# Kernel tuning notes

Hardware: AMD Instinct MI355X
Metric: run time of the kernel (lower is better)

The kernel has to match this reference:

```python
import jax, jax.numpy as jnp
import numpy as np

B, S, N = 64, 256, 512


def setup_inputs() -> dict:
    key = jax.random.key(0)
    ks = jax.random.split(key, 8)
    x = jax.random.normal(ks[0], (B, S, N), dtype=jnp.float32)
    # sparse adjacency, no self loops (module assumes adj has no self-loop)
    adj = (jax.random.uniform(ks[1], (N, N)) < 0.05).astype(jnp.float32)
    adj = adj * (1.0 - jnp.eye(N, dtype=jnp.float32))
    W = jax.random.uniform(ks[2], (N, N), dtype=jnp.float32)  # torch.rand init
    parent_node_weigh = jax.random.uniform(ks[3], (N,), dtype=jnp.float32)
    bound = 1.0 / np.sqrt(N)  # torch Linear default init
    Wq_w = jax.random.uniform(ks[4], (N, N), minval=-bound, maxval=bound, dtype=jnp.float32)
    Wq_b = jax.random.uniform(ks[5], (N,), minval=-bound, maxval=bound, dtype=jnp.float32)
    Wk_w = jax.random.uniform(ks[6], (N, N), minval=-bound, maxval=bound, dtype=jnp.float32)
    Wk_b = jax.random.uniform(ks[7], (N,), minval=-bound, maxval=bound, dtype=jnp.float32)
    return {"x": x, "adj": adj, "W": W, "parent_node_weigh": parent_node_weigh,
            "Wq_w": Wq_w, "Wq_b": Wq_b, "Wk_w": Wk_w, "Wk_b": Wk_b}


def reference(x, adj, W, parent_node_weigh, Wq_w, Wq_b, Wk_w, Wk_b):
    # x: (B,S,N). Q,K = Linear(x).permute(0,2,1) -> (B,N,S)
    Q = jnp.einsum('bsk,nk->bns', x, Wq_w) + Wq_b[None, :, None]
    K = jnp.einsum('bsk,nk->bns', x, Wk_w) + Wk_b[None, :, None]
    xt = jnp.transpose(x, (0, 2, 1))  # (B,N,S)
    n = adj.shape[0]
    # Algebraic equivalent of the repeat/mask/matmul/bmm chain:
    # Att[b,m,n] = adj[m,n] * sum_j W[m,j] * adj[j,n] * <K[b,j,:], Q[b,n,:]>
    S_kq = jnp.einsum('bjs,bns->bjn', K, Q)  # (B,N,N)
    Att = adj * jnp.einsum('mj,bjn->bmn', W, adj[:, :, None].transpose(2, 0, 1)[0][None] * S_kq if False else adj[None, :, :] * S_kq)
    Att = Att + jnp.diag(parent_node_weigh)[None, :, :]
    cycle_adj = jnp.eye(n, dtype=adj.dtype) + adj
    Att = jax.nn.softmax(Att, axis=1) * cycle_adj  # softmax over dim=1 (torch dim=1)
    agg_x = jnp.einsum('bmn,bms->bns', Att, xt)  # Att^T @ x
    return (agg_x, Att)
```

## Files before the change

### kernel.cpp

```cpp
#include <hip/hip_runtime.h>
#include <hip/hip_fp16.h>
#include <cstdint>
#include <cmath>

#define BB 64
#define SS 256
#define NN 512
#define MAXC 64

typedef float f32x4 __attribute__((ext_vector_type(4)));
typedef _Float16 half8 __attribute__((ext_vector_type(8)));

__device__ __forceinline__ unsigned short f2h(float f) {
  return __half_as_ushort(__float2half(f));
}
__device__ __forceinline__ float h2f(unsigned short u) {
  return __half2float(__ushort_as_half(u));
}

__device__ __forceinline__ void gload_lds16(const void* g, void* s) {
  __builtin_amdgcn_global_load_lds(
      (const __attribute__((address_space(1))) uint32_t*)g,
      (__attribute__((address_space(3))) uint32_t*)s, 16, 0, 0);
}

__global__ __launch_bounds__(256) void k_prep0(const float* __restrict__ adj,
                                               int* __restrict__ col_idx,
                                               int* __restrict__ col_cnt,
                                               const float* __restrict__ Wq,
                                               const float* __restrict__ Wk,
                                               unsigned short* __restrict__ Wqp,
                                               unsigned short* __restrict__ Wkp) {
  if (blockIdx.x < 128) {
    const int n = blockIdx.x * 4 + (threadIdx.x >> 6);
    const int lane = threadIdx.x & 63;
    int cnt = 0;
    for (int m0 = 0; m0 < NN; m0 += 64) {
      const int m = m0 + lane;
      const float a = adj[(size_t)m * NN + n];
      unsigned long long mask = __ballot(a != 0.0f);
      const int prefix = __popcll(mask & ((1ull << lane) - 1ull));
      if (a != 0.0f && cnt + prefix < MAXC) col_idx[n * MAXC + cnt + prefix] = m;
      cnt += __popcll(mask);
    }
    if (lane == 0) col_cnt[n] = (cnt > MAXC) ? MAXC : cnt;
  } else {
    const int n = blockIdx.x - 128;
    const int half = threadIdx.x >> 7;
    const float* src = half ? Wk : Wq;
    unsigned short* dst = half ? Wkp : Wqp;
    const int k = (threadIdx.x & 127) * 4;
    float4 v = *(const float4*)(src + (size_t)n * NN + k);
    ushort4 o;
    o.x = f2h(v.x); o.y = f2h(v.y); o.z = f2h(v.z); o.w = f2h(v.w);
    *(ushort4*)(dst + (size_t)n * 512 + k) = o;
  }
}

__global__ __launch_bounds__(256) void k_wsub(const float* __restrict__ W,
                                              const int* __restrict__ col_idx,
                                              const int* __restrict__ col_cnt,
                                              int* __restrict__ col_off,
                                              float* __restrict__ Wsub) {
  const int n = blockIdx.x;
  const int t = threadIdx.x;
  const int wave = t >> 6, lane = t & 63;
  __shared__ int lsh[MAXC];
  __shared__ int preSh;
  const int c = col_cnt[n];
  if (wave == 0) {
    int pre = 0;
#pragma unroll
    for (int i0 = 0; i0 < NN; i0 += 64) {
      const int i = i0 + lane;
      const int cc = col_cnt[i];
      pre += (i < n) ? cc * cc : 0;
    }
#pragma unroll
    for (int off = 32; off; off >>= 1) pre += __shfl_xor(pre, off);
    if (lane == 0) { col_off[n] = pre; preSh = pre; }
    if (lane < c) lsh[lane] = col_idx[n * MAXC + lane];
  }
  __syncthreads();
  if (lane < c) {
    const float* Wm = W + (size_t)lsh[lane] * NN;
    float* dst = Wsub + preSh + lane;
    for (int ji = wave; ji < c; ji += 4)
      dst[(size_t)ji * c] = Wm[lsh[ji]];
  }
}

__global__ __launch_bounds__(256) void k_xprep(const float* __restrict__ x,
                                               unsigned short* __restrict__ xp,
                                               float* __restrict__ Att) {
  const int t = threadIdx.x;
  const size_t base = ((size_t)blockIdx.x * 256 + t) * 4;
  float4 v = *(const float4*)(x + base);
  ushort4 o;
  o.x = f2h(v.x); o.y = f2h(v.y); o.z = f2h(v.z); o.w = f2h(v.w);
  *(ushort4*)(xp + base) = o;
  f32x4* dst = (f32x4*)(Att + (size_t)blockIdx.x * 2048);
  const f32x4 z = (f32x4)0.0f;
  dst[t] = z;
  dst[t + 256] = z;
}

__global__ __launch_bounds__(256, 2) void k_lin2(const unsigned short* __restrict__ Wqp,
                                                 const unsigned short* __restrict__ Wkp,
                                                 const float* __restrict__ bq,
                                                 const float* __restrict__ bk,
                                                 const unsigned short* __restrict__ xp,
                                                 unsigned short* __restrict__ Qt,
                                                 unsigned short* __restrict__ Kt) {
  __shared__ __align__(16) char sm[49152];
  const int t = threadIdx.x;
  const int w = t >> 6, l = t & 63;
  const int id = blockIdx.x;
  const int xcd = id & 7, sub = id >> 3;
  const int bn0 = (xcd * 16 + (sub >> 2)) * 128;
  const int bm0 = (sub & 3) * 128;

  const int swz = (((l & 3) ^ ((l >> 3) & 3))) * 16;
  const char* srcb[6];
  char* dstb[6];
#pragma unroll
  for (int i = 0; i < 6; i++) {
    const int ch = w * 6 + i;
    const int panel = ch >> 3, rowgrp = ch & 7;
    const int row = rowgrp * 16 + (l >> 2);
    const char* g0 = (panel == 0) ? (const char*)Wqp
                   : (panel == 1) ? (const char*)Wkp : (const char*)xp;
    const int gr = ((panel == 2) ? bn0 : bm0) + row;
    srcb[i] = g0 + (size_t)gr * 1024 + swz;
    dstb[i] = sm + panel * 8192 + rowgrp * 1024 + l * 16;
  }

  const int fr = l & 15, fg = l >> 4;
  const int mrow = (w >> 1) * 64, ncol = (w & 1) * 64;
  const int slot = (fg ^ ((fr >> 1) & 3)) * 16;
  int offQ[4], offK[4], offB[4];
#pragma unroll
  for (int fm = 0; fm < 4; fm++) {
    offQ[fm] = (mrow + fm * 16 + fr) * 64 + slot;
    offK[fm] = 8192 + (mrow + fm * 16 + fr) * 64 + slot;
    offB[fm] = 16384 + (ncol + fm * 16 + fr) * 64 + slot;
  }

  f32x4 accq[4][4], acck[4][4];
#pragma unroll
  for (int i = 0; i < 4; i++)
#pragma unroll
    for (int j = 0; j < 4; j++) { accq[i][j] = (f32x4)0.0f; acck[i][j] = (f32x4)0.0f; }

#pragma unroll
  for (int i = 0; i < 6; i++) gload_lds16(srcb[i], dstb[i]);
  __syncthreads();

  int cur = 0;
  for (int kk = 0; kk < 16; kk++) {
    if (kk + 1 < 16) {
      const int ko = (kk + 1) * 64;
      const int boff = (cur ^ 1) * 24576;
#pragma unroll
      for (int i = 0; i < 6; i++)
        gload_lds16(srcb[i] + ko, dstb[i] + boff);
    }
    const char* base = sm + cur * 24576;
    half8 afq[4], afk[4];
#pragma unroll
    for (int fm = 0; fm < 4; fm++) {
      afq[fm] = *(const half8*)(base + offQ[fm]);
      afk[fm] = *(const half8*)(base + offK[fm]);
    }
#pragma unroll
    for (int fn = 0; fn < 4; fn++) {
      const half8 bv = *(const half8*)(base + offB[fn]);
#pragma unroll
      for (int fm = 0; fm < 4; fm++) {
        accq[fm][fn] = __builtin_amdgcn_mfma_f32_16x16x32_f16(afq[fm], bv, accq[fm][fn], 0, 0, 0);
        acck[fm][fn] = __builtin_amdgcn_mfma_f32_16x16x32_f16(afk[fm], bv, acck[fm][fn], 0, 0, 0);
      }
    }
    __syncthreads();
    cur ^= 1;
  }

  const int b = bn0 >> 8;
  const int sbase = (bn0 & 255) + ncol;
#pragma unroll
  for (int fm = 0; fm < 4; fm++) {
#pragma unroll
    for (int q = 0; q < 4; q++) {
      const int n = bm0 + mrow + fm * 16 + fg * 4 + q;
      const float bvq = bq[n];
      const float bvk = bk[n];
#pragma unroll
      for (int fn = 0; fn < 4; fn++) {
        const int s = sbase + fn * 16 + fr;
        Qt[((size_t)b * NN + n) * SS + s] = f2h(accq[fm][fn][q] + bvq);
        Kt[((size_t)b * NN + n) * SS + s] = f2h(acck[fm][fn][q] + bvk);
      }
    }
  }
}

__global__ __launch_bounds__(256, 2) void k_gram(const unsigned short* __restrict__ Qt,
                                                 const unsigned short* __restrict__ Kt,
                                                 unsigned short* __restrict__ ST) {
  __shared__ __align__(16) char sm[32768];
  const int t = threadIdx.x;
  const int w = t >> 6, l = t & 63;
  const int id = blockIdx.x;
  const int xcd = id & 7, rest = id >> 3;
  const int batch = (xcd << 3) + (rest >> 4);
  const int tile = rest & 15;
  const int m0 = (tile >> 2) * 128;
  const int n0 = (tile & 3) * 128;

  const int swz = (((l & 3) ^ ((l >> 3) & 3))) * 16;
  const char* srcb[4];
  char* dstb[4];
#pragma unroll
  for (int i = 0; i < 4; i++) {
    const int ch = w * 4 + i;
    const int panel = ch >> 3, rowgrp = ch & 7;
    const int row = rowgrp * 16 + (l >> 2);
    const char* g0 = panel ? (const char*)Kt : (const char*)Qt;
    const int gr = (panel ? n0 : m0) + row;
    srcb[i] = g0 + ((size_t)batch * 512 + gr) * 512 + swz;
    dstb[i] = sm + panel * 8192 + rowgrp * 1024 + l * 16;
  }

  const int fr = l & 15, fg = l >> 4;
  const int mrow = (w >> 1) * 64, ncol = (w & 1) * 64;
  const int slot = (fg ^ ((fr >> 1) & 3)) * 16;
  int offA[4], offB[4];
#pragma unroll
  for (int fm = 0; fm < 4; fm++) {
    offA[fm] = (mrow + fm * 16 + fr) * 64 + slot;
    offB[fm] = 8192 + (ncol + fm * 16 + fr) * 64 + slot;
  }

  f32x4 acc[4][4];
#pragma unroll
  for (int i = 0; i < 4; i++)
#pragma unroll
    for (int j = 0; j < 4; j++) acc[i][j] = (f32x4)0.0f;

#pragma unroll
  for (int i = 0; i < 4; i++) gload_lds16(srcb[i], dstb[i]);
  __syncthreads();

  int cur = 0;
  for (int kk = 0; kk < 8; kk++) {
    if (kk + 1 < 8) {
      const int ko = (kk + 1) * 64;
      const int boff = (cur ^ 1) * 16384;
#pragma unroll
      for (int i = 0; i < 4; i++)
        gload_lds16(srcb[i] + ko, dstb[i] + boff);
    }
    const char* base = sm + cur * 16384;
    half8 af[4];
#pragma unroll
    for (int fm = 0; fm < 4; fm++)
      af[fm] = *(const half8*)(base + offA[fm]);
#pragma unroll
    for (int fn = 0; fn < 4; fn++) {
      const half8 bv = *(const half8*)(base + offB[fn]);
#pragma unroll
      for (int fm = 0; fm < 4; fm++)
        acc[fm][fn] = __builtin_amdgcn_mfma_f32_16x16x32_f16(af[fm], bv, acc[fm][fn], 0, 0, 0);
    }
    __syncthreads();
    cur ^= 1;
  }

  unsigned short* STb = ST + (size_t)batch * NN * NN;
#pragma unroll
  for (int fm = 0; fm < 4; fm++) {
#pragma unroll
    for (int q = 0; q < 4; q++) {
      const int n = m0 + mrow + fm * 16 + fg * 4 + q;
#pragma unroll
      for (int fn = 0; fn < 4; fn++) {
        const int j = n0 + ncol + fn * 16 + fr;
        STb[(size_t)n * NN + j] = f2h(acc[fm][fn][q]);
      }
    }
  }
}

__global__ __launch_bounds__(256) void k_fused(const unsigned short* __restrict__ ST,
                                               const float* __restrict__ Wsub,
                                               const float* __restrict__ pnw,
                                               const int* __restrict__ col_idx,
                                               const int* __restrict__ col_cnt,
                                               const int* __restrict__ col_off,
                                               float* __restrict__ Att,
                                               unsigned short* __restrict__ Att2) {
  const int id = blockIdx.x;
  const int xcd = id & 7;
  const int r = id >> 3;
  const int n = r & 511;
  const int bgrp = r >> 9;
  const int t = threadIdx.x;
  const int wave = t >> 6, lane = t & 63;
  const int b = (xcd << 3) + (bgrp << 2) + wave;

  __shared__ int   lsh[MAXC + 1];
  __shared__ float Wsh[MAXC * MAXC];
  __shared__ float vsh[4][MAXC];
  __shared__ unsigned short ush[4][NN];

  const int c = col_cnt[n];

  unsigned short stv = 0;
  if (lane < c) {
    const int myIdx = col_idx[n * MAXC + lane];
    stv = ST[((size_t)b * NN + n) * NN + myIdx];
  }

#pragma unroll
  for (int j = 0; j < 8; j++) ush[wave][lane * 8 + j] = 0;

  if (t < c) lsh[t] = col_idx[n * MAXC + t];
  if (t == c) lsh[c] = n;
  {
    const int cc = c * c;
    const float* Wp = Wsub + col_off[n];
    for (int i = t; i < cc; i += 256) Wsh[i] = Wp[i];
  }
  __syncthreads();

  if (lane < c) vsh[wave][lane] = h2f(stv);

  float aval = 0.0f;
  if (lane < c) {
    for (int ji = 0; ji < c; ji++)
      aval += Wsh[ji * c + lane] * vsh[wave][ji];
  }

  const float dlg = pnw[n];
  float mval = (lane < c) ? aval : -INFINITY;
#pragma unroll
  for (int off = 32; off; off >>= 1) mval = fmaxf(mval, __shfl_xor(mval, off));
  const float colmax = fmaxf(mval, fmaxf(dlg, 0.0f));
  const float e = (lane < c) ? __expf(aval - colmax) : 0.0f;
  float sum = e;
#pragma unroll
  for (int off = 32; off; off >>= 1) sum += __shfl_xor(sum, off);
  const float denom = sum + __expf(dlg - colmax)
                    + (float)(NN - c - 1) * __expf(-colmax);
  const float inv = 1.0f / denom;

  float* Acol = Att + (size_t)b * NN * NN + n;
  if (lane < c) {
    const float attv = e * inv;
    Acol[(size_t)lsh[lane] * NN] = attv;
    ush[wave][lsh[lane]] = f2h(attv);
  }
  if (lane == c) {
    const float dv = __expf(dlg - colmax) * inv;
    Acol[(size_t)n * NN] = dv;
    ush[wave][n] = f2h(dv);
  }

  uint32_t pk[4];
#pragma unroll
  for (int j = 0; j < 4; j++) {
    const uint32_t lo = ush[wave][lane * 8 + j * 2];
    const uint32_t hi = ush[wave][lane * 8 + j * 2 + 1];
    pk[j] = lo | (hi << 16);
  }
  uint4 o = make_uint4(pk[0], pk[1], pk[2], pk[3]);
  *(uint4*)((char*)Att2 + ((size_t)b * NN + n) * 1024 + lane * 16) = o;
}

__global__ __launch_bounds__(256, 2) void k_agg(const unsigned short* __restrict__ Att2,
                                                const unsigned short* __restrict__ xp,
                                                float* __restrict__ agg) {
  __shared__ __align__(16) char sm[32768];
  const int t = threadIdx.x;
  const int w = t >> 6, l = t & 63;
  const int id = blockIdx.x;
  const int xcd = id & 7, rest = id >> 3;
  const int batch = (xcd << 3) + (rest >> 3);
  const int tile = rest & 7;
  const int m0 = (tile >> 1) * 128;
  const int s0 = (tile & 1) * 128;

  const int swz = (((l & 3) ^ ((l >> 3) & 3))) * 16;
  const char* srcb[4];
  char* dstb[4];
#pragma unroll
  for (int i = 0; i < 4; i++) {
    const int ch = w * 4 + i;
    const int panel = ch >> 3, rowgrp = ch & 7;
    const int row = rowgrp * 16 + (l >> 2);
    const char* g0 = panel ? (const char*)xp : (const char*)Att2;
    const size_t gr = panel ? ((size_t)batch * SS + s0 + row)
                            : ((size_t)batch * NN + m0 + row);
    srcb[i] = g0 + gr * 1024 + swz;
    dstb[i] = sm + panel * 8192 + rowgrp * 1024 + l * 16;
  }

  const int fr = l & 15, fg = l >> 4;
  const int mrow = (w >> 1) * 64, ncol = (w & 1) * 64;
  const int slot = (fg ^ ((fr >> 1) & 3)) * 16;
  int offA[4], offB[4];
#pragma unroll
  for (int fm = 0; fm < 4; fm++) {
    offA[fm] = (mrow + fm * 16 + fr) * 64 + slot;
    offB[fm] = 8192 + (ncol + fm * 16 + fr) * 64 + slot;
  }

  f32x4 acc[4][4];
#pragma unroll
  for (int i = 0; i < 4; i++)
#pragma unroll
    for (int j = 0; j < 4; j++) acc[i][j] = (f32x4)0.0f;

#pragma unroll
  for (int i = 0; i < 4; i++) gload_lds16(srcb[i], dstb[i]);
  __syncthreads();

  int cur = 0;
  for (int kk = 0; kk < 16; kk++) {
    if (kk + 1 < 16) {
      const int ko = (kk + 1) * 64;
      const int boff = (cur ^ 1) * 16384;
#pragma unroll
      for (int i = 0; i < 4; i++)
        gload_lds16(srcb[i] + ko, dstb[i] + boff);
    }
    const char* base = sm + cur * 16384;
    half8 af[4];
#pragma unroll
    for (int fm = 0; fm < 4; fm++)
      af[fm] = *(const half8*)(base + offA[fm]);
#pragma unroll
    for (int fn = 0; fn < 4; fn++) {
      const half8 bv = *(const half8*)(base + offB[fn]);
#pragma unroll
      for (int fm = 0; fm < 4; fm++)
        acc[fm][fn] = __builtin_amdgcn_mfma_f32_16x16x32_f16(af[fm], bv, acc[fm][fn], 0, 0, 0);
    }
    __syncthreads();
    cur ^= 1;
  }

  float* ab = agg + (size_t)batch * NN * SS;
#pragma unroll
  for (int fm = 0; fm < 4; fm++) {
#pragma unroll
    for (int q = 0; q < 4; q++) {
      const int n = m0 + mrow + fm * 16 + fg * 4 + q;
#pragma unroll
      for (int fn = 0; fn < 4; fn++) {
        const int s = s0 + ncol + fn * 16 + fr;
        ab[(size_t)n * SS + s] = acc[fm][fn][q];
      }
    }
  }
}

extern "C" void kernel_launch(void* const* d_in, const int* in_sizes, int n_in,
                              void* d_out, int out_size, void* d_ws, size_t ws_size,
                              hipStream_t stream) {
  const float* x    = (const float*)d_in[0];
  const float* adj  = (const float*)d_in[1];
  const float* W    = (const float*)d_in[2];
  const float* pnw  = (const float*)d_in[3];
  const float* Wq_w = (const float*)d_in[4];
  const float* Wq_b = (const float*)d_in[5];
  const float* Wk_w = (const float*)d_in[6];
  const float* Wk_b = (const float*)d_in[7];

  float* agg = (float*)d_out;
  float* Att = (float*)d_out + (size_t)BB * NN * SS;

  char* p = (char*)d_ws;
  unsigned short* xp  = (unsigned short*)p; p += (size_t)BB * SS * 512 * 2;
  unsigned short* Wqp = (unsigned short*)p; p += (size_t)NN * 512 * 2;
  unsigned short* Wkp = (unsigned short*)p; p += (size_t)NN * 512 * 2;
  unsigned short* Qt  = (unsigned short*)p; p += (size_t)BB * NN * SS * 2;
  unsigned short* Kt  = (unsigned short*)p; p += (size_t)BB * NN * SS * 2;
  unsigned short* ST  = (unsigned short*)p; p += (size_t)BB * NN * NN * 2;
  unsigned short* At2 = (unsigned short*)p; p += (size_t)BB * NN * NN * 2;
  float* Wsub = (float*)p; p += (size_t)NN * MAXC * MAXC * 4;
  int* col_idx = (int*)p; p += (size_t)NN * MAXC * 4;
  int* col_cnt = (int*)p; p += NN * 4;
  int* col_off = (int*)p;

  k_prep0<<<dim3(640), dim3(256), 0, stream>>>(adj, col_idx, col_cnt,
                                               Wq_w, Wk_w, Wqp, Wkp);
  k_wsub<<<dim3(NN), dim3(256), 0, stream>>>(W, col_idx, col_cnt, col_off, Wsub);
  k_xprep<<<dim3(8192), dim3(256), 0, stream>>>(x, xp, Att);

  k_lin2<<<dim3(512), dim3(256), 0, stream>>>(Wqp, Wkp, Wq_b, Wk_b, xp, Qt, Kt);
  k_gram<<<dim3(1024), dim3(256), 0, stream>>>(Qt, Kt, ST);
  k_fused<<<dim3(8192), dim3(256), 0, stream>>>(ST, Wsub, pnw,
                                                col_idx, col_cnt, col_off,
                                                Att, At2);
  k_agg<<<dim3(512), dim3(256), 0, stream>>>(At2, xp, agg);
}
```

Baseline: 111.3 us.

## Merge x-prep into prep kernel and widen gram/agg tiles to 128x256

Folds the x fp16 conversion and Att zeroing into the prep kernel, removing one launch. Doubles the N-dimension tile in the gram and aggregation GEMMs to 128x256 (8 fragments per wave), halving their grid sizes and reusing the A panel across more columns. In exchange the accumulator register count doubles and LDS use rises to 48KB. This may cut occupancy, and 256 blocks for k_agg could underfill the GPU's compute units.

```diff
diff --git a/kernel.cpp b/kernel.cpp
--- a/kernel.cpp
+++ b/kernel.cpp
@@ -24,15 +24,19 @@
       (__attribute__((address_space(3))) uint32_t*)s, 16, 0, 0);
 }
 
-__global__ __launch_bounds__(256) void k_prep0(const float* __restrict__ adj,
-                                               int* __restrict__ col_idx,
-                                               int* __restrict__ col_cnt,
-                                               const float* __restrict__ Wq,
-                                               const float* __restrict__ Wk,
-                                               unsigned short* __restrict__ Wqp,
-                                               unsigned short* __restrict__ Wkp) {
-  if (blockIdx.x < 128) {
-    const int n = blockIdx.x * 4 + (threadIdx.x >> 6);
+__global__ __launch_bounds__(256) void k_prep(const float* __restrict__ adj,
+                                              int* __restrict__ col_idx,
+                                              int* __restrict__ col_cnt,
+                                              const float* __restrict__ Wq,
+                                              const float* __restrict__ Wk,
+                                              unsigned short* __restrict__ Wqp,
+                                              unsigned short* __restrict__ Wkp,
+                                              const float* __restrict__ x,
+                                              unsigned short* __restrict__ xp,
+                                              float* __restrict__ Att) {
+  const int bid = blockIdx.x;
+  if (bid < 128) {
+    const int n = bid * 4 + (threadIdx.x >> 6);
     const int lane = threadIdx.x & 63;
     int cnt = 0;
     for (int m0 = 0; m0 < NN; m0 += 64) {
@@ -44,8 +48,8 @@
       cnt += __popcll(mask);
     }
     if (lane == 0) col_cnt[n] = (cnt > MAXC) ? MAXC : cnt;
-  } else {
-    const int n = blockIdx.x - 128;
+  } else if (bid < 640) {
+    const int n = bid - 128;
     const int half = threadIdx.x >> 7;
     const float* src = half ? Wk : Wq;
     unsigned short* dst = half ? Wkp : Wqp;
@@ -54,6 +58,18 @@
     ushort4 o;
     o.x = f2h(v.x); o.y = f2h(v.y); o.z = f2h(v.z); o.w = f2h(v.w);
     *(ushort4*)(dst + (size_t)n * 512 + k) = o;
+  } else {
+    const int q = bid - 640;
+    const int t = threadIdx.x;
+    const size_t base = ((size_t)q * 256 + t) * 4;
+    float4 v = *(const float4*)(x + base);
+    ushort4 o;
+    o.x = f2h(v.x); o.y = f2h(v.y); o.z = f2h(v.z); o.w = f2h(v.w);
+    *(ushort4*)(xp + base) = o;
+    f32x4* dst = (f32x4*)(Att + (size_t)q * 2048);
+    const f32x4 z = (f32x4)0.0f;
+    dst[t] = z;
+    dst[t + 256] = z;
   }
 }
 
@@ -88,21 +104,6 @@
     for (int ji = wave; ji < c; ji += 4)
       dst[(size_t)ji * c] = Wm[lsh[ji]];
   }
-}
-
-__global__ __launch_bounds__(256) void k_xprep(const float* __restrict__ x,
-                                               unsigned short* __restrict__ xp,
-                                               float* __restrict__ Att) {
-  const int t = threadIdx.x;
-  const size_t base = ((size_t)blockIdx.x * 256 + t) * 4;
-  float4 v = *(const float4*)(x + base);
-  ushort4 o;
-  o.x = f2h(v.x); o.y = f2h(v.y); o.z = f2h(v.z); o.w = f2h(v.w);
-  *(ushort4*)(xp + base) = o;
-  f32x4* dst = (f32x4*)(Att + (size_t)blockIdx.x * 2048);
-  const f32x4 z = (f32x4)0.0f;
-  dst[t] = z;
-  dst[t + 256] = z;
 }
 
 __global__ __launch_bounds__(256, 2) void k_lin2(const unsigned short* __restrict__ Wqp,
@@ -207,66 +208,68 @@
 __global__ __launch_bounds__(256, 2) void k_gram(const unsigned short* __restrict__ Qt,
                                                  const unsigned short* __restrict__ Kt,
                                                  unsigned short* __restrict__ ST) {
-  __shared__ __align__(16) char sm[32768];
+  __shared__ __align__(16) char sm[49152];
   const int t = threadIdx.x;
   const int w = t >> 6, l = t & 63;
   const int id = blockIdx.x;
   const int xcd = id & 7, rest = id >> 3;
-  const int batch = (xcd << 3) + (rest >> 4);
-  const int tile = rest & 15;
-  const int m0 = (tile >> 2) * 128;
-  const int n0 = (tile & 3) * 128;
+  const int batch = (xcd << 3) + (rest >> 3);
+  const int tile = rest & 7;
+  const int m0 = (tile >> 1) * 128;
+  const int j0 = (tile & 1) * 256;
 
   const int swz = (((l & 3) ^ ((l >> 3) & 3))) * 16;
-  const char* srcb[4];
-  char* dstb[4];
-#pragma unroll
-  for (int i = 0; i < 4; i++) {
-    const int ch = w * 4 + i;
-    const int panel = ch >> 3, rowgrp = ch & 7;
+  const char* srcb[6];
+  char* dstb[6];
+#pragma unroll
+  for (int i = 0; i < 6; i++) {
+    const int ch = w * 6 + i;
+    const int panel = (ch >= 8) ? 1 : 0;
+    const int rowgrp = panel ? (ch - 8) : ch;
     const int row = rowgrp * 16 + (l >> 2);
     const char* g0 = panel ? (const char*)Kt : (const char*)Qt;
-    const int gr = (panel ? n0 : m0) + row;
+    const int gr = (panel ? j0 : m0) + row;
     srcb[i] = g0 + ((size_t)batch * 512 + gr) * 512 + swz;
     dstb[i] = sm + panel * 8192 + rowgrp * 1024 + l * 16;
   }
 
   const int fr = l & 15, fg = l >> 4;
-  const int mrow = (w >> 1) * 64, ncol = (w & 1) * 64;
+  const int mrow = (w >> 1) * 64, jcol = (w & 1) * 128;
   const int slot = (fg ^ ((fr >> 1) & 3)) * 16;
-  int offA[4], offB[4];
-#pragma unroll
-  for (int fm = 0; fm < 4; fm++) {
+  int offA[4], offB[8];
+#pragma unroll
+  for (int fm = 0; fm < 4; fm++)
     offA[fm] = (mrow + fm * 16 + fr) * 64 + slot;
-    offB[fm] = 8192 + (ncol + fm * 16 + fr) * 64 + slot;
-  }
-
-  f32x4 acc[4][4];
+#pragma unroll
+  for (int fn = 0; fn < 8; fn++)
+    offB[fn] = 8192 + (jcol + fn * 16 + fr) * 64 + slot;
+
+  f32x4 acc[4][8];
 #pragma unroll
   for (int i = 0; i < 4; i++)
 #pragma unroll
-    for (int j = 0; j < 4; j++) acc[i][j] = (f32x4)0.0f;
-
-#pragma unroll
-  for (int i = 0; i < 4; i++) gload_lds16(srcb[i], dstb[i]);
+    for (int j = 0; j < 8; j++) acc[i][j] = (f32x4)0.0f;
+
+#pragma unroll
+  for (int i = 0; i < 6; i++) gload_lds16(srcb[i], dstb[i]);
   __syncthreads();
 
   int cur = 0;
   for (int kk = 0; kk < 8; kk++) {
     if (kk + 1 < 8) {
       const int ko = (kk + 1) * 64;
-      const int boff = (cur ^ 1) * 16384;
-#pragma unroll
-      for (int i = 0; i < 4; i++)
+      const int boff = (cur ^ 1) * 24576;
+#pragma unroll
+      for (int i = 0; i < 6; i++)
         gload_lds16(srcb[i] + ko, dstb[i] + boff);
     }
-    const char* base = sm + cur * 16384;
+    const char* base = sm + cur * 24576;
     half8 af[4];
 #pragma unroll
     for (int fm = 0; fm < 4; fm++)
       af[fm] = *(const half8*)(base + offA[fm]);
 #pragma unroll
-    for (int fn = 0; fn < 4; fn++) {
+    for (int fn = 0; fn < 8; fn++) {
       const half8 bv = *(const half8*)(base + offB[fn]);
 #pragma unroll
       for (int fm = 0; fm < 4; fm++)
@@ -283,8 +286,8 @@
     for (int q = 0; q < 4; q++) {
       const int n = m0 + mrow + fm * 16 + fg * 4 + q;
 #pragma unroll
-      for (int fn = 0; fn < 4; fn++) {
-        const int j = n0 + ncol + fn * 16 + fr;
+      for (int fn = 0; fn < 8; fn++) {
+        const int j = j0 + jcol + fn * 16 + fr;
         STb[(size_t)n * NN + j] = f2h(acc[fm][fn][q]);
       }
     }
@@ -380,67 +383,67 @@
 __global__ __launch_bounds__(256, 2) void k_agg(const unsigned short* __restrict__ Att2,
                                                 const unsigned short* __restrict__ xp,
                                                 float* __restrict__ agg) {
-  __shared__ __align__(16) char sm[32768];
+  __shared__ __align__(16) char sm[49152];
   const int t = threadIdx.x;
   const int w = t >> 6, l = t & 63;
   const int id = blockIdx.x;
   const int xcd = id & 7, rest = id >> 3;
-  const int batch = (xcd << 3) + (rest >> 3);
-  const int tile = rest & 7;
-  const int m0 = (tile >> 1) * 128;
-  const int s0 = (tile & 1) * 128;
+  const int batch = (xcd << 3) + (rest >> 2);
+  const int m0 = (rest & 3) * 128;
 
   const int swz = (((l & 3) ^ ((l >> 3) & 3))) * 16;
-  const char* srcb[4];
-  char* dstb[4];
-#pragma unroll
-  for (int i = 0; i < 4; i++) {
-    const int ch = w * 4 + i;
-    const int panel = ch >> 3, rowgrp = ch & 7;
+  const char* srcb[6];
+  char* dstb[6];
+#pragma unroll
+  for (int i = 0; i < 6; i++) {
+    const int ch = w * 6 + i;
+    const int panel = (ch >= 8) ? 1 : 0;
+    const int rowgrp = panel ? (ch - 8) : ch;
     const int row = rowgrp * 16 + (l >> 2);
     const char* g0 = panel ? (const char*)xp : (const char*)Att2;
-    const size_t gr = panel ? ((size_t)batch * SS + s0 + row)
+    const size_t gr = panel ? ((size_t)batch * SS + row)
                             : ((size_t)batch * NN + m0 + row);
     srcb[i] = g0 + gr * 1024 + swz;
     dstb[i] = sm + panel * 8192 + rowgrp * 1024 + l * 16;
   }
 
   const int fr = l & 15, fg = l >> 4;
-  const int mrow = (w >> 1) * 64, ncol = (w & 1) * 64;
+  const int mrow = (w >> 1) * 64, scol = (w & 1) * 128;
   const int slot = (fg ^ ((fr >> 1) & 3)) * 16;
-  int offA[4], offB[4];
-#pragma unroll
-  for (int fm = 0; fm < 4; fm++) {
+  int offA[4], offB[8];
+#pragma unroll
+  for (int fm = 0; fm < 4; fm++)
     offA[fm] = (mrow + fm * 16 + fr) * 64 + slot;
-    offB[fm] = 8192 + (ncol + fm * 16 + fr) * 64 + slot;
-  }
-
-  f32x4 acc[4][4];
+#pragma unroll
+  for (int fn = 0; fn < 8; fn++)
+    offB[fn] = 8192 + (scol + fn * 16 + fr) * 64 + slot;
+
+  f32x4 acc[4][8];
 #pragma unroll
   for (int i = 0; i < 4; i++)
 #pragma unroll
-    for (int j = 0; j < 4; j++) acc[i][j] = (f32x4)0.0f;
-
-#pragma unroll
-  for (int i = 0; i < 4; i++) gload_lds16(srcb[i], dstb[i]);
+    for (int j = 0; j < 8; j++) acc[i][j] = (f32x4)0.0f;
+
+#pragma unroll
+  for (int i = 0; i < 6; i++) gload_lds16(srcb[i], dstb[i]);
   __syncthreads();
 
   int cur = 0;
   for (int kk = 0; kk < 16; kk++) {
     if (kk + 1 < 16) {
       const int ko = (kk + 1) * 64;
-      const int boff = (cur ^ 1) * 16384;
-#pragma unroll
-      for (int i = 0; i < 4; i++)
+      const int boff = (cur ^ 1) * 24576;
+#pragma unroll
+      for (int i = 0; i < 6; i++)
         gload_lds16(srcb[i] + ko, dstb[i] + boff);
     }
-    const char* base = sm + cur * 16384;
+    const char* base = sm + cur * 24576;
     half8 af[4];
 #pragma unroll
     for (int fm = 0; fm < 4; fm++)
       af[fm] = *(const half8*)(base + offA[fm]);
 #pragma unroll
-    for (int fn = 0; fn < 4; fn++) {
+    for (int fn = 0; fn < 8; fn++) {
       const half8 bv = *(const half8*)(base + offB[fn]);
 #pragma unroll
       for (int fm = 0; fm < 4; fm++)
@@ -457,8 +460,8 @@
     for (int q = 0; q < 4; q++) {
       const int n = m0 + mrow + fm * 16 + fg * 4 + q;
 #pragma unroll
-      for (int fn = 0; fn < 4; fn++) {
-        const int s = s0 + ncol + fn * 16 + fr;
+      for (int fn = 0; fn < 8; fn++) {
+        const int s = scol + fn * 16 + fr;
         ab[(size_t)n * SS + s] = acc[fm][fn][q];
       }
     }
@@ -493,15 +496,15 @@
   int* col_cnt = (int*)p; p += NN * 4;
   int* col_off = (int*)p;
 
-  k_prep0<<<dim3(640), dim3(256), 0, stream>>>(adj, col_idx, col_cnt,
-                                               Wq_w, Wk_w, Wqp, Wkp);
+  k_prep<<<dim3(8832), dim3(256), 0, stream>>>(adj, col_idx, col_cnt,
+                                               Wq_w, Wk_w, Wqp, Wkp,
+                                               x, xp, Att);
   k_wsub<<<dim3(NN), dim3(256), 0, stream>>>(W, col_idx, col_cnt, col_off, Wsub);
-  k_xprep<<<dim3(8192), dim3(256), 0, stream>>>(x, xp, Att);
 
   k_lin2<<<dim3(512), dim3(256), 0, stream>>>(Wqp, Wkp, Wq_b, Wk_b, xp, Qt, Kt);
-  k_gram<<<dim3(1024), dim3(256), 0, stream>>>(Qt, Kt, ST);
+  k_gram<<<dim3(512), dim3(256), 0, stream>>>(Qt, Kt, ST);
   k_fused<<<dim3(8192), dim3(256), 0, stream>>>(ST, Wsub, pnw,
                                                 col_idx, col_cnt, col_off,
                                                 Att, At2);
-  k_agg<<<dim3(512), dim3(256), 0, stream>>>(At2, xp, agg);
-}
+  k_agg<<<dim3(256), dim3(256), 0, stream>>>(At2, xp, agg);
+}
```

Result: no change. 110.1 us (-1.0%).
